# Performance work log

Measured on AMD Instinct MI355X. Metric: run time of the kernel, lower is better.

The kernel has to match this reference:

```python
import jax, jax.numpy as jnp
import numpy as np

M_MARGIN = 0.25
GAMMA = 256.0
NEG_INF = jnp.float32(-1e30)


def setup_inputs() -> dict:
    key = jax.random.key(0)
    k1, k2 = jax.random.split(key)
    feature = jax.random.normal(k1, (8192, 128), dtype=jnp.float32)
    label = jax.random.randint(k2, (8192,), 0, 64, dtype=jnp.int64)
    return {"feature": feature, "label": label}


def reference(feature, label):
    # F.normalize: L2-normalize rows (eps=1e-12)
    norm = jnp.maximum(jnp.linalg.norm(feature, axis=1, keepdims=True), 1e-12)
    f = feature / norm
    sim = f @ f.T  # [N, N]
    N = sim.shape[0]

    same = label[:, None] == label[None, :]
    triu = jnp.triu(jnp.ones((N, N), dtype=bool), k=1)
    pos_mask = same & triu
    neg_mask = (~same) & triu

    sim_d = jax.lax.stop_gradient(sim)  # .detach() in original
    ap = jnp.maximum(-sim_d + 1.0 + M_MARGIN, 0.0)
    an = jnp.maximum(sim_d + M_MARGIN, 0.0)
    delta_p = 1.0 - M_MARGIN
    delta_n = M_MARGIN

    logit_p = -ap * (sim - delta_p) * GAMMA
    logit_n = an * (sim - delta_n) * GAMMA

    # boolean-gather + logsumexp == masked logsumexp (fixed shapes, jit-friendly)
    lse_p = jax.nn.logsumexp(jnp.where(pos_mask, logit_p, NEG_INF))
    lse_n = jax.nn.logsumexp(jnp.where(neg_mask, logit_n, NEG_INF))

    return jax.nn.softplus(lse_n + lse_p)
```

## Files before the change

### kernel.cpp

```cpp
#include <hip/hip_runtime.h>
#include <hip/hip_bf16.h>
#include <math.h>

#define NROW 8192
#define DIM  128
#define BM   128
#define BN   128
#define NT   (NROW / BM)
#define NTILES ((NT * (NT + 1)) / 2)

typedef __bf16 bf16x8 __attribute__((ext_vector_type(8)));
typedef float  f32x4  __attribute__((ext_vector_type(4)));

#define G2      369.3299304675746f
#define NEGBIG  (-3.0e38f)
#define NOFF    2000.0f

__global__ __launch_bounds__(256)
void prep_kernel(const float* __restrict__ f, __hip_bfloat16* __restrict__ fhi) {
    int row  = blockIdx.x * 4 + (threadIdx.x >> 6);
    int lane = threadIdx.x & 63;
    float2 v = ((const float2*)(f + (size_t)row * DIM))[lane];
    float ss = v.x * v.x + v.y * v.y;
    #pragma unroll
    for (int off = 32; off; off >>= 1) ss += __shfl_xor(ss, off, 64);
    float inv = 1.0f / fmaxf(sqrtf(ss), 1e-12f);
    __hip_bfloat162 hv;
    hv.x = __float2bfloat16(v.x * inv);
    hv.y = __float2bfloat16(v.y * inv);
    ((__hip_bfloat162*)(fhi + (size_t)row * DIM))[lane] = hv;
}

__global__ __launch_bounds__(256, 4)
void sim_kernel(const __hip_bfloat16* __restrict__ fhi,
                const int* __restrict__ lab,
                float4* __restrict__ blockRes) {
    const int tid  = threadIdx.x;
    const int w    = tid >> 6;
    const int lane = tid & 63;
    const int lrow = lane & 15;
    const int lk   = lane >> 4;

    int bid = blockIdx.x;
    int tr = (int)((129.0f - sqrtf(16641.0f - 8.0f * (float)bid)) * 0.5f);
    while (tr > 0 && bid < tr * NT - (tr * (tr - 1)) / 2) --tr;
    while (bid >= (tr + 1) * NT - ((tr + 1) * tr) / 2) ++tr;
    const int tc = tr + (bid - (tr * NT - (tr * (tr - 1)) / 2));

    const int rowBase = tr * BM;
    const int colBase = tc * BN;

    __shared__ __align__(16) char smem[4 * 16384];
    __shared__ int labA[BM];
    __shared__ int labB[BN];
    __shared__ float red[4][4];

    if (tid < BM) labA[tid] = lab[rowBase + tid];
    else          labB[tid - BM] = lab[colBase + (tid - BM)];

    f32x4 acc[4][4];
    #pragma unroll
    for (int mi = 0; mi < 4; ++mi)
        #pragma unroll
        for (int ni = 0; ni < 4; ++ni) acc[mi][ni] = (f32x4){0.f, 0.f, 0.f, 0.f};

    const int mrow0 = (w >> 1) * 64;
    const int ncol0 = (w & 1) * 64;

    const int rsub = lane >> 3;
    const int kbs  = 16 * ((lane & 7) ^ rsub);

    #pragma unroll
    for (int t = 0; t < 16; ++t) {
        int sg  = w * 16 + t;
        int arr = sg >> 4;
        int s16 = sg & 15;
        int kc  = arr >> 1;
        char* ldsb = smem + arr * 16384 + s16 * 1024;
        int grow = ((arr & 1) ? colBase : rowBase) + s16 * 8 + rsub;
        const char* g = (const char*)fhi + (size_t)grow * 256 + kc * 128 + kbs;
        __builtin_amdgcn_global_load_lds(
            (const __attribute__((address_space(1))) void*)g,
            (__attribute__((address_space(3))) void*)ldsb, 16, 0, 0);
    }
    __syncthreads();

    #pragma unroll
    for (int kc = 0; kc < 2; ++kc) {
        const char* As = smem + kc * 32768;
        const char* Bs = As + 16384;
        #pragma unroll
        for (int c = 0; c < 2; ++c) {
            int kb = c * 64 + lk * 16;
            bf16x8 bfr[4];
            #pragma unroll
            for (int ni = 0; ni < 4; ++ni) {
                int rb = ncol0 + ni * 16 + lrow;
                bfr[ni] = *(const bf16x8*)(Bs + rb * 128 + (kb ^ ((rb & 7) << 4)));
            }
            #pragma unroll
            for (int mi = 0; mi < 4; ++mi) {
                int ra = mrow0 + mi * 16 + lrow;
                bf16x8 afr = *(const bf16x8*)(As + ra * 128 + (kb ^ ((ra & 7) << 4)));
                #pragma unroll
                for (int ni = 0; ni < 4; ++ni)
                    acc[mi][ni] = __builtin_amdgcn_mfma_f32_16x16x32_bf16(afr, bfr[ni], acc[mi][ni], 0, 0, 0);
            }
        }
    }

    const float Ppos = -2.0f * G2;
    const float Qpos = 0.9375f * G2;
    const float Qneg = -0.0625f * G2 - NOFF;
    float mall = NEGBIG, mneg = NEGBIG;
    const bool diag = (tr == tc);

    int lbv[4];
    #pragma unroll
    for (int ni = 0; ni < 4; ++ni) lbv[ni] = labB[ncol0 + ni * 16 + lrow];

    #pragma unroll
    for (int mi = 0; mi < 4; ++mi) {
        const int il0 = mrow0 + mi * 16 + lk * 4;
        int4 la4 = *(const int4*)&labA[il0];
        const int la[4] = {la4.x, la4.y, la4.z, la4.w};
        #pragma unroll
        for (int ni = 0; ni < 4; ++ni) {
            const int jl = ncol0 + ni * 16 + lrow;
            #pragma unroll
            for (int r = 0; r < 4; ++r) {
                float s = acc[mi][ni][r];
                bool pos = (la[r] == lbv[ni]);
                float P  = pos ? Ppos : 0.0f;
                float Qc = pos ? Qpos : Qneg;
                float base = fmaf(G2, s * s, fmaf(P, s, Qc));
                bool keep = pos || (s > -0.25f);
                float x = keep ? base : -NOFF;
                if (diag) x = (jl > il0 + r) ? x : NEGBIG;
                mall = fmaxf(mall, x);
                float xn = pos ? NEGBIG : x;
                mneg = fmaxf(mneg, xn);
                acc[mi][ni][r] = x;
            }
        }
    }

    #pragma unroll
    for (int off = 32; off; off >>= 1) {
        mall = fmaxf(mall, __shfl_xor(mall, off, 64));
        mneg = fmaxf(mneg, __shfl_xor(mneg, off, 64));
    }
    if (lane == 0) { red[w][0] = mall; red[w][1] = mneg; }
    __syncthreads();
    const float mar = fmaxf(fmaxf(red[0][0], red[1][0]), fmaxf(red[2][0], red[3][0]));
    const float mnr = fmaxf(fmaxf(red[0][1], red[1][1]), fmaxf(red[2][1], red[3][1]));
    const float Mp  = (mar > -1000.f) ? mar : 0.f;
    const float Mn2 = (mnr > -2500.f) ? mnr : -1000.f;

    float sp = 0.f, sn = 0.f;
    #pragma unroll
    for (int mi = 0; mi < 4; ++mi)
        #pragma unroll
        for (int ni = 0; ni < 4; ++ni)
            #pragma unroll
            for (int r = 0; r < 4; ++r) {
                float x = acc[mi][ni][r];
                sp += __builtin_amdgcn_exp2f(x - Mp);
                float xm = (x > -1000.f) ? NEGBIG : x;
                sn += __builtin_amdgcn_exp2f(xm - Mn2);
            }

    #pragma unroll
    for (int off = 32; off; off >>= 1) {
        sp += __shfl_xor(sp, off, 64);
        sn += __shfl_xor(sn, off, 64);
    }
    __syncthreads();
    if (lane == 0) { red[w][2] = sp; red[w][3] = sn; }
    __syncthreads();
    if (tid == 0) {
        float Sp = red[0][2] + red[1][2] + red[2][2] + red[3][2];
        float Sn = red[0][3] + red[1][3] + red[2][3] + red[3][3];
        blockRes[bid] = make_float4(Mp, Sp, Mn2, Sn);
    }
}

__device__ __forceinline__ void merge2(float& m, float& s, float mo, float so) {
    float M = fmaxf(m, mo);
    s = s * __builtin_amdgcn_exp2f(m - M) + so * __builtin_amdgcn_exp2f(mo - M);
    m = M;
}

__global__ __launch_bounds__(256)
void finalize_kernel(const float4* __restrict__ blockRes, float* __restrict__ out) {
    __shared__ float red[4][4];
    int tid = threadIdx.x;
    float mp = NEGBIG, sp = 0.f, mn = NEGBIG, sn = 0.f;
    for (int i = tid; i < NTILES; i += 256) {
        float4 v = blockRes[i];
        merge2(mp, sp, v.x, v.y);
        merge2(mn, sn, v.z, v.w);
    }
    #pragma unroll
    for (int off = 32; off; off >>= 1) {
        float mo = __shfl_xor(mp, off, 64), so = __shfl_xor(sp, off, 64);
        merge2(mp, sp, mo, so);
        float mo2 = __shfl_xor(mn, off, 64), so2 = __shfl_xor(sn, off, 64);
        merge2(mn, sn, mo2, so2);
    }
    int wv = tid >> 6;
    if ((tid & 63) == 0) {
        red[wv][0] = mp; red[wv][1] = sp; red[wv][2] = mn; red[wv][3] = sn;
    }
    __syncthreads();
    if (tid == 0) {
        mp = red[0][0]; sp = red[0][1]; mn = red[0][2]; sn = red[0][3];
        #pragma unroll
        for (int q = 1; q < 4; ++q) {
            merge2(mp, sp, red[q][0], red[q][1]);
            merge2(mn, sn, red[q][2], red[q][3]);
        }
        const double LN2 = 0.6931471805599453;
        double lse_p = ((double)mp + log2((double)sp)) * LN2;
        double lse_n = ((double)mn + (double)NOFF + log2((double)sn)) * LN2;
        double xx = lse_p + lse_n;
        double r = (xx > 30.0) ? xx : log1p(exp(xx));
        out[0] = (float)r;
    }
}

extern "C" void kernel_launch(void* const* d_in, const int* in_sizes, int n_in,
                              void* d_out, int out_size, void* d_ws, size_t ws_size,
                              hipStream_t stream) {
    const float* f   = (const float*)d_in[0];
    const int*   lab = (const int*)d_in[1];
    float*  out      = (float*)d_out;

    __hip_bfloat16* fhi = (__hip_bfloat16*)d_ws;
    float4* blockRes    = (float4*)((char*)d_ws + 4u * 1024 * 1024);

    prep_kernel<<<NROW / 4, 256, 0, stream>>>(f, fhi);
    sim_kernel<<<NTILES, 256, 0, stream>>>(fhi, lab, blockRes);
    finalize_kernel<<<1, 256, 0, stream>>>(blockRes, out);
}
```

Before: 48.67 us.

## Use 64x128 tiles over the upper triangle and halve exp2 work

The sim kernel now uses 64-row by 128-column tiles, which roughly doubles the block count (4160) and halves per-thread accumulators. The upper-triangle tile index mapping is rewritten for the rectangular tiling, and the diagonal mask uses global indices on the edge tiles. K-chunks are loaded into a smaller 24KB LDS buffer in two stages with extra syncs. The epilogue now computes a single exp2 per element, picking the max by class, instead of two. The goals are better occupancy and load balance and fewer transcendental instructions, at the cost of less operand reuse per tile and more synchronization.

```diff
diff --git a/kernel.cpp b/kernel.cpp
--- a/kernel.cpp
+++ b/kernel.cpp
@@ -4,10 +4,11 @@
 
 #define NROW 8192
 #define DIM  128
-#define BM   128
+#define BM   64
 #define BN   128
-#define NT   (NROW / BM)
-#define NTILES ((NT * (NT + 1)) / 2)
+#define TM   (NROW / BM)
+#define TN   (NROW / BN)
+#define NTILES 4160
 
 typedef __bf16 bf16x8 __attribute__((ext_vector_type(8)));
 typedef float  f32x4  __attribute__((ext_vector_type(4)));
@@ -29,6 +30,12 @@
     hv.x = __float2bfloat16(v.x * inv);
     hv.y = __float2bfloat16(v.y * inv);
     ((__hip_bfloat162*)(fhi + (size_t)row * DIM))[lane] = hv;
+}
+
+__device__ __forceinline__ int tstart(int tr) {
+    int m = tr >> 1;
+    int f = m * m - ((tr & 1) ? 0 : m);
+    return 64 * tr - f;
 }
 
 __global__ __launch_bounds__(256, 4)
@@ -42,91 +49,90 @@
     const int lk   = lane >> 4;
 
     int bid = blockIdx.x;
-    int tr = (int)((129.0f - sqrtf(16641.0f - 8.0f * (float)bid)) * 0.5f);
-    while (tr > 0 && bid < tr * NT - (tr * (tr - 1)) / 2) --tr;
-    while (bid >= (tr + 1) * NT - ((tr + 1) * tr) / 2) ++tr;
-    const int tc = tr + (bid - (tr * NT - (tr * (tr - 1)) / 2));
+    float sa = fmaxf(16384.f - 4.f * (float)bid, 0.f);
+    int tr = 128 - (int)sqrtf(sa);
+    if (tr > 127) tr = 127;
+    if (tr < 0) tr = 0;
+    while (tr > 0 && bid < tstart(tr)) --tr;
+    while (bid >= tstart(tr + 1)) ++tr;
+    const int tc = (tr >> 1) + (bid - tstart(tr));
 
     const int rowBase = tr * BM;
     const int colBase = tc * BN;
 
-    __shared__ __align__(16) char smem[4 * 16384];
+    __shared__ __align__(16) char smem[24 * 1024];
     __shared__ int labA[BM];
     __shared__ int labB[BN];
     __shared__ float red[4][4];
 
-    if (tid < BM) labA[tid] = lab[rowBase + tid];
-    else          labB[tid - BM] = lab[colBase + (tid - BM)];
-
-    f32x4 acc[4][4];
+    if (tid < BM)                 labA[tid] = lab[rowBase + tid];
+    else if (tid < BM + BN)       labB[tid - BM] = lab[colBase + (tid - BM)];
+
+    f32x4 acc[4][2];
     #pragma unroll
     for (int mi = 0; mi < 4; ++mi)
         #pragma unroll
-        for (int ni = 0; ni < 4; ++ni) acc[mi][ni] = (f32x4){0.f, 0.f, 0.f, 0.f};
-
-    const int mrow0 = (w >> 1) * 64;
-    const int ncol0 = (w & 1) * 64;
+        for (int ni = 0; ni < 2; ++ni) acc[mi][ni] = (f32x4){0.f, 0.f, 0.f, 0.f};
+
+    const int ncol0 = w * 32;
 
     const int rsub = lane >> 3;
     const int kbs  = 16 * ((lane & 7) ^ rsub);
 
-    #pragma unroll
-    for (int t = 0; t < 16; ++t) {
-        int sg  = w * 16 + t;
-        int arr = sg >> 4;
-        int s16 = sg & 15;
-        int kc  = arr >> 1;
-        char* ldsb = smem + arr * 16384 + s16 * 1024;
-        int grow = ((arr & 1) ? colBase : rowBase) + s16 * 8 + rsub;
-        const char* g = (const char*)fhi + (size_t)grow * 256 + kc * 128 + kbs;
-        __builtin_amdgcn_global_load_lds(
-            (const __attribute__((address_space(1))) void*)g,
-            (__attribute__((address_space(3))) void*)ldsb, 16, 0, 0);
-    }
-    __syncthreads();
-
-    #pragma unroll
     for (int kc = 0; kc < 2; ++kc) {
-        const char* As = smem + kc * 32768;
-        const char* Bs = As + 16384;
+        #pragma unroll
+        for (int t = 0; t < 6; ++t) {
+            int seg = w * 6 + t;
+            char* ldsb = smem + seg * 1024;
+            int grow = (seg < 8) ? (rowBase + (seg & 7) * 8 + rsub)
+                                 : (colBase + (seg - 8) * 8 + rsub);
+            const char* g = (const char*)fhi + (size_t)grow * 256 + kc * 128 + kbs;
+            __builtin_amdgcn_global_load_lds(
+                (const __attribute__((address_space(1))) void*)g,
+                (__attribute__((address_space(3))) void*)ldsb, 16, 0, 0);
+        }
+        __syncthreads();
+
+        const char* As = smem;
+        const char* Bs = smem + 8192;
         #pragma unroll
         for (int c = 0; c < 2; ++c) {
             int kb = c * 64 + lk * 16;
-            bf16x8 bfr[4];
-            #pragma unroll
-            for (int ni = 0; ni < 4; ++ni) {
+            bf16x8 bfr[2];
+            #pragma unroll
+            for (int ni = 0; ni < 2; ++ni) {
                 int rb = ncol0 + ni * 16 + lrow;
                 bfr[ni] = *(const bf16x8*)(Bs + rb * 128 + (kb ^ ((rb & 7) << 4)));
             }
             #pragma unroll
             for (int mi = 0; mi < 4; ++mi) {
-                int ra = mrow0 + mi * 16 + lrow;
+                int ra = mi * 16 + lrow;
                 bf16x8 afr = *(const bf16x8*)(As + ra * 128 + (kb ^ ((ra & 7) << 4)));
                 #pragma unroll
-                for (int ni = 0; ni < 4; ++ni)
+                for (int ni = 0; ni < 2; ++ni)
                     acc[mi][ni] = __builtin_amdgcn_mfma_f32_16x16x32_bf16(afr, bfr[ni], acc[mi][ni], 0, 0, 0);
             }
         }
+        __syncthreads();
     }
 
     const float Ppos = -2.0f * G2;
     const float Qpos = 0.9375f * G2;
     const float Qneg = -0.0625f * G2 - NOFF;
     float mall = NEGBIG, mneg = NEGBIG;
-    const bool diag = (tr == tc);
-
-    int lbv[4];
-    #pragma unroll
-    for (int ni = 0; ni < 4; ++ni) lbv[ni] = labB[ncol0 + ni * 16 + lrow];
+    const bool edge = (tc == (tr >> 1));
+
+    int lbv[2];
+    #pragma unroll
+    for (int ni = 0; ni < 2; ++ni) lbv[ni] = labB[ncol0 + ni * 16 + lrow];
 
     #pragma unroll
     for (int mi = 0; mi < 4; ++mi) {
-        const int il0 = mrow0 + mi * 16 + lk * 4;
-        int4 la4 = *(const int4*)&labA[il0];
+        int4 la4 = *(const int4*)&labA[mi * 16 + lk * 4];
         const int la[4] = {la4.x, la4.y, la4.z, la4.w};
         #pragma unroll
-        for (int ni = 0; ni < 4; ++ni) {
-            const int jl = ncol0 + ni * 16 + lrow;
+        for (int ni = 0; ni < 2; ++ni) {
+            const int jg = colBase + ncol0 + ni * 16 + lrow;
             #pragma unroll
             for (int r = 0; r < 4; ++r) {
                 float s = acc[mi][ni][r];
@@ -136,10 +142,12 @@
                 float base = fmaf(G2, s * s, fmaf(P, s, Qc));
                 bool keep = pos || (s > -0.25f);
                 float x = keep ? base : -NOFF;
-                if (diag) x = (jl > il0 + r) ? x : NEGBIG;
+                if (edge) {
+                    int ig = rowBase + mi * 16 + lk * 4 + r;
+                    x = (jg > ig) ? x : NEGBIG;
+                }
                 mall = fmaxf(mall, x);
-                float xn = pos ? NEGBIG : x;
-                mneg = fmaxf(mneg, xn);
+                mneg = fmaxf(mneg, pos ? NEGBIG : x);
                 acc[mi][ni][r] = x;
             }
         }
@@ -161,13 +169,16 @@
     #pragma unroll
     for (int mi = 0; mi < 4; ++mi)
         #pragma unroll
-        for (int ni = 0; ni < 4; ++ni)
+        for (int ni = 0; ni < 2; ++ni)
             #pragma unroll
             for (int r = 0; r < 4; ++r) {
                 float x = acc[mi][ni][r];
-                sp += __builtin_amdgcn_exp2f(x - Mp);
-                float xm = (x > -1000.f) ? NEGBIG : x;
-                sn += __builtin_amdgcn_exp2f(xm - Mn2);
+                bool p2 = (x > -1000.f);
+                float Ms = p2 ? Mp : Mn2;
+                float e = __builtin_amdgcn_exp2f(x - Ms);
+                float ep = p2 ? e : 0.f;
+                sp += ep;
+                sn += (e - ep);
             }
 
     #pragma unroll
```

Result: faster. 44.98 us (-7.6%).
